# Performance work log

Measured on AMD Instinct MI355X. Metric: run time of the kernel, lower is better.

## Reference

```python
import jax, jax.numpy as jnp
import numpy as np
import math

N_HEADS = 8
D_MODEL = 512
ACTUAL_N = 16
ACTUAL_CH = 64
SEQ = ACTUAL_N * ACTUAL_CH  # 1024
BATCH = 8


def _alibi_slopes(n):
    # n_heads=8 is a power of two, so only the power-of-2 branch is needed
    start = 2.0 ** (-(2.0 ** (-(math.log2(n) - 3))))
    return [start * (start ** i) for i in range(n)]


def setup_inputs() -> dict:
    key = jax.random.key(0)
    ks = jax.random.split(key, 9)
    d = D_MODEL
    w = 0.02  # init scale for weights
    return {
        "Q": jax.random.normal(ks[0], (BATCH, SEQ, d), jnp.float32),
        "Wq": jax.random.normal(ks[1], (d, d), jnp.float32) * w,
        "bq": jnp.zeros((d,), jnp.float32),
        "Wk": jax.random.normal(ks[2], (d, d), jnp.float32) * w,
        "bk": jnp.zeros((d,), jnp.float32),
        "Wv": jax.random.normal(ks[3], (d, d), jnp.float32) * w,
        "bv": jnp.zeros((d,), jnp.float32),
        "Wo": jax.random.normal(ks[4], (d, d), jnp.float32) * w,
        "bo": jnp.zeros((d,), jnp.float32),
        "mask": jnp.ones((SEQ, SEQ), bool),
        "actual_N": ACTUAL_N,
        "actual_ch": ACTUAL_CH,
    }


def reference(Q, Wq, bq, Wk, bk, Wv, bv, Wo, bo, mask, actual_N, actual_ch):
    bs, S, d = Q.shape
    H = N_HEADS
    dk = d // H
    scale = dk ** -0.5  # lsa=False -> frozen scalar

    # QKV projections (K = V = Q, self-attention path), [bs, H, S, dk]
    q = (Q @ Wq.T + bq).reshape(bs, S, H, dk).transpose(0, 2, 1, 3)
    k = (Q @ Wk.T + bk).reshape(bs, S, H, dk).transpose(0, 2, 1, 3)
    v = (Q @ Wv.T + bv).reshape(bs, S, H, dk).transpose(0, 2, 1, 3)

    scores = jnp.einsum('bhqd,bhkd->bhqk', q, k) * scale  # [bs,H,S,S]

    # ALiBi-style bias: per-head slope * tiled (-|i-j|) distance block
    slopes = jnp.asarray(_alibi_slopes(H), jnp.float32)[:, None, None]  # [H,1,1]
    pos = jnp.arange(actual_N)
    dist = (-jnp.abs(pos[:, None] - pos[None, :])).astype(jnp.float32)  # [N,N]
    bias = slopes * jnp.tile(dist, (actual_ch, actual_ch))  # [H,S,S]
    scores = scores + bias

    # mask: True = keep (masked_fill on ~mask)
    scores = jnp.where(mask[None, None, :, :], scores, -jnp.inf)

    attn = jax.nn.softmax(scores, axis=-1)  # dropout=0 (eval)
    out = jnp.einsum('bhqk,bhkd->bhqd', attn, v)  # [bs,H,S,dk]
    out = out.transpose(0, 2, 1, 3).reshape(bs, S, H * dk)
    out = out @ Wo.T + bo
    return (out, attn)
```

## Files before the change

kernel.cpp:

```cpp
#include <hip/hip_runtime.h>
#include <cmath>


namespace {
constexpr int SEQ = 1024;
constexpr int DM  = 512;
constexpr int NH  = 8;
constexpr int DK  = 64;
constexpr float SCALE = 0.125f;
constexpr size_t QKV_ELEMS = (size_t)8 * NH * SEQ * DK;
}

typedef __attribute__((ext_vector_type(8))) short short8_t;
typedef __attribute__((ext_vector_type(4))) float f32x4_t;
typedef __attribute__((ext_vector_type(2))) unsigned u32x2_t;
typedef __attribute__((ext_vector_type(4))) unsigned short ushort4_t;

__device__ inline unsigned bf16h(float x) {
  union { float f; unsigned u; } c; c.f = x;
  return (c.u + 0x7FFFu + ((c.u >> 16) & 1u)) >> 16;
}
__device__ inline float bf16f(unsigned h) {
  union { unsigned u; float f; } c; c.u = h << 16; return c.f;
}

#define GLOAD_LDS16(g, l) __builtin_amdgcn_global_load_lds( \
    (const __attribute__((address_space(1))) void*)(g), \
    (__attribute__((address_space(3))) void*)(l), 16, 0, 0)

__global__ __launch_bounds__(256) void k0_convert(
    const float* __restrict__ X,
    const float* __restrict__ Wq, const float* __restrict__ Wk,
    const float* __restrict__ Wv, const float* __restrict__ Wo,
    unsigned short* __restrict__ Xh, unsigned short* __restrict__ Xl,
    unsigned short* __restrict__ Wh, unsigned short* __restrict__ Wl,
    unsigned short* __restrict__ Woh, unsigned short* __restrict__ Wol)
{
  const size_t gi = ((size_t)blockIdx.x * 256 + threadIdx.x) * 8;
  const float* src; unsigned short* dh; unsigned short* dl; size_t off;
  if (gi < 4194304) { src = X; dh = Xh; dl = Xl; off = gi; }
  else {
    const size_t r = gi - 4194304;
    const int sec = (int)(r >> 18);
    off = r & 262143;
    if (sec == 0)      { src = Wq; dh = Wh;          dl = Wl; }
    else if (sec == 1) { src = Wk; dh = Wh + 262144; dl = Wl + 262144; }
    else if (sec == 2) { src = Wv; dh = Wh + 524288; dl = Wl + 524288; }
    else               { src = Wo; dh = Woh;         dl = Wol; }
  }
  const float4 f0 = *(const float4*)&src[off];
  const float4 f1 = *(const float4*)&src[off + 4];
  const float v[8] = {f0.x, f0.y, f0.z, f0.w, f1.x, f1.y, f1.z, f1.w};
  short8_t hv, lv;
#pragma unroll
  for (int j = 0; j < 8; ++j) {
    const unsigned hh = bf16h(v[j]);
    hv[j] = (short)hh;
    lv[j] = (short)bf16h(v[j] - bf16f(hh));
  }
  *(short8_t*)&dh[off] = hv;
  *(short8_t*)&dl[off] = lv;
}

__device__ inline int swz64(int row, int col16) {
  return row * 64 + (col16 ^ (((row >> 1) & 3) << 4));
}

__global__ __launch_bounds__(256, 3) void k1_gemm(
    const unsigned short* __restrict__ Xh, const unsigned short* __restrict__ Xl,
    const unsigned short* __restrict__ Wh, const unsigned short* __restrict__ Wl,
    const float* __restrict__ bq, const float* __restrict__ bk,
    const float* __restrict__ bv,
    unsigned short* __restrict__ Qh, unsigned short* __restrict__ Ql,
    unsigned short* __restrict__ Kh, unsigned short* __restrict__ Kl,
    unsigned short* __restrict__ VTh, unsigned short* __restrict__ VTl)
{
  const int z = blockIdx.z;
  const int m0 = blockIdx.x * 128, n0 = blockIdx.y * 128;
  const unsigned short* __restrict__ Bph = Wh + (size_t)z * 262144;
  const unsigned short* __restrict__ Bpl = Wl + (size_t)z * 262144;
  const float* bias = (z == 0) ? bq : (z == 1) ? bk : bv;

  __shared__ __align__(16) char sm[32768];

  const int tid = threadIdx.x;
  const int w = tid >> 6, lane = tid & 63, lq = lane & 15, g = lane >> 4;
  const int wm = w >> 1, wn = w & 1;
  const int srow = tid >> 2, schunk = (tid & 3) * 16;

  f32x4_t acc[4][4];
#pragma unroll
  for (int i = 0; i < 4; ++i)
#pragma unroll
    for (int j = 0; j < 4; ++j) acc[i][j] = (f32x4_t){0.f, 0.f, 0.f, 0.f};

  for (int k0 = 0; k0 < DM; k0 += 32) {
    const int kc = k0 + (schunk >> 1);
    const short8_t a0h = *(const short8_t*)&Xh[(size_t)(m0 + srow)      * DM + kc];
    const short8_t a1h = *(const short8_t*)&Xh[(size_t)(m0 + srow + 64) * DM + kc];
    const short8_t a0l = *(const short8_t*)&Xl[(size_t)(m0 + srow)      * DM + kc];
    const short8_t a1l = *(const short8_t*)&Xl[(size_t)(m0 + srow + 64) * DM + kc];
    const short8_t b0h = *(const short8_t*)&Bph[(size_t)(n0 + srow)      * DM + kc];
    const short8_t b1h = *(const short8_t*)&Bph[(size_t)(n0 + srow + 64) * DM + kc];
    const short8_t b0l = *(const short8_t*)&Bpl[(size_t)(n0 + srow)      * DM + kc];
    const short8_t b1l = *(const short8_t*)&Bpl[(size_t)(n0 + srow + 64) * DM + kc];
    __syncthreads();
    *(short8_t*)(sm +         swz64(srow,      schunk)) = a0h;
    *(short8_t*)(sm +         swz64(srow + 64, schunk)) = a1h;
    *(short8_t*)(sm +  8192 + swz64(srow,      schunk)) = a0l;
    *(short8_t*)(sm +  8192 + swz64(srow + 64, schunk)) = a1l;
    *(short8_t*)(sm + 16384 + swz64(srow,      schunk)) = b0h;
    *(short8_t*)(sm + 16384 + swz64(srow + 64, schunk)) = b1h;
    *(short8_t*)(sm + 24576 + swz64(srow,      schunk)) = b0l;
    *(short8_t*)(sm + 24576 + swz64(srow + 64, schunk)) = b1l;
    __syncthreads();

    short8_t ah[4], al[4], bh_[4], bl_[4];
#pragma unroll
    for (int mf = 0; mf < 4; ++mf) {
      const int rowA = wm * 64 + mf * 16 + lq;
      ah[mf] = *(const short8_t*)(sm +        swz64(rowA, g * 16));
      al[mf] = *(const short8_t*)(sm + 8192 + swz64(rowA, g * 16));
    }
#pragma unroll
    for (int nf = 0; nf < 4; ++nf) {
      const int rowB = wn * 64 + nf * 16 + lq;
      bh_[nf] = *(const short8_t*)(sm + 16384 + swz64(rowB, g * 16));
      bl_[nf] = *(const short8_t*)(sm + 24576 + swz64(rowB, g * 16));
    }
#pragma unroll
    for (int mf = 0; mf < 4; ++mf)
#pragma unroll
      for (int nf = 0; nf < 4; ++nf) {
        acc[mf][nf] = __builtin_amdgcn_mfma_f32_16x16x32_bf16(ah[mf], bh_[nf], acc[mf][nf], 0, 0, 0);
        acc[mf][nf] = __builtin_amdgcn_mfma_f32_16x16x32_bf16(al[mf], bh_[nf], acc[mf][nf], 0, 0, 0);
        acc[mf][nf] = __builtin_amdgcn_mfma_f32_16x16x32_bf16(ah[mf], bl_[nf], acc[mf][nf], 0, 0, 0);
      }
  }

  if (z <= 1) {
    unsigned short* Ph = (z == 0) ? Qh : Kh;
    unsigned short* Pl = (z == 0) ? Ql : Kl;
#pragma unroll
    for (int mf = 0; mf < 4; ++mf)
#pragma unroll
      for (int nf = 0; nf < 4; ++nf) {
        const int N = n0 + wn * 64 + nf * 16 + lq;
        const int h = N >> 6, dd = N & 63;
        const float bs = bias[N];
#pragma unroll
        for (int r = 0; r < 4; ++r) {
          const int M = m0 + wm * 64 + mf * 16 + g * 4 + r;
          const int b = M >> 10, s = M & 1023;
          const float val = acc[mf][nf][r] + bs;
          const unsigned hi = bf16h(val);
          const size_t o = ((size_t)((b * 8 + h) * 1024 + s)) * 64 + dd;
          Ph[o] = (unsigned short)hi;
          Pl[o] = (unsigned short)bf16h(val - bf16f(hi));
        }
      }
  } else {
#pragma unroll
    for (int mf = 0; mf < 4; ++mf)
#pragma unroll
      for (int nf = 0; nf < 4; ++nf) {
        const int N = n0 + wn * 64 + nf * 16 + lq;
        const int h = N >> 6, dd = N & 63;
        const float bs = bias[N];
        const int M0 = m0 + wm * 64 + mf * 16 + g * 4;
        const int b = M0 >> 10, s = M0 & 1023;
        ushort4_t hv, lv;
#pragma unroll
        for (int r = 0; r < 4; ++r) {
          const float val = acc[mf][nf][r] + bs;
          const unsigned hi = bf16h(val);
          hv[r] = (unsigned short)hi;
          lv[r] = (unsigned short)bf16h(val - bf16f(hi));
        }
        const size_t o = ((size_t)((b * 8 + h) * 64 + dd)) * 1024 + s;
        *(ushort4_t*)&VTh[o] = hv;
        *(ushort4_t*)&VTl[o] = lv;
      }
  }
}

__global__ __launch_bounds__(512, 2) void k_attn(
    const unsigned short* __restrict__ Qhp, const unsigned short* __restrict__ Qlp,
    const unsigned short* __restrict__ Khp, const unsigned short* __restrict__ Klp,
    const unsigned short* __restrict__ VTh, const unsigned short* __restrict__ VTl,
    float* __restrict__ attn,
    unsigned short* __restrict__ HOh, unsigned short* __restrict__ HOl)
{
  __shared__ __align__(16) char smem[49664];
  float* rsm = (float*)(smem + 49152);

  const int bid = blockIdx.x;
  const int swz = (bid & 7) * 256 + (bid >> 3);
  const int bh = swz >> 5, qt = swz & 31;
  const int hh = bh & 7;
  const float slope = exp2f(-(float)(hh + 1));

  const int tid = threadIdx.x, w = tid >> 6, lane = tid & 63;
  const int lq = lane & 15, g = lane >> 4;
  const int qhalf = w >> 2, kq = w & 3;

  const size_t qkBase = (size_t)bh * (SEQ * DK);

  short8_t qfh[2], qfl[2];
  {
    const size_t qr = qkBase + (size_t)(qt * 32 + qhalf * 16 + lq) * DK;
#pragma unroll
    for (int ks = 0; ks < 2; ++ks) {
      qfh[ks] = *(const short8_t*)&Qhp[qr + ks * 32 + g * 8];
      qfl[ks] = *(const short8_t*)&Qlp[qr + ks * 32 + g * 8];
    }
  }

  float bias[4];
#pragma unroll
  for (int r = 0; r < 4; ++r) {
    const int d = lq - (g * 4 + r);
    bias[r] = -slope * (float)(d < 0 ? -d : d);
  }

  const int srow8 = tid >> 3;
  const int sc    = ((tid & 7) ^ (srow8 & 7)) * 8;

  const int krow = kq * 16 + lq;
  const int kro  = krow * 128;
  const int kc0  = (g ^ (krow & 7)) << 4;
  const int kc1  = ((4 + g) ^ (krow & 7)) << 4;

  f32x4_t e_[16];
  float rs = 0.f;

  {
    const size_t kb0 = qkBase + (size_t)srow8 * DK + sc;
    GLOAD_LDS16(&Khp[kb0], smem + tid * 16);
    GLOAD_LDS16(&Klp[kb0], smem + 8192 + tid * 16);
    const size_t kb1 = qkBase + (size_t)(64 + srow8) * DK + sc;
    GLOAD_LDS16(&Khp[kb1], smem + 16384 + tid * 16);
    GLOAD_LDS16(&Klp[kb1], smem + 16384 + 8192 + tid * 16);
  }

#pragma unroll
  for (int hp = 0; hp < 16; ++hp) {
    if (hp < 15) asm volatile("s_waitcnt vmcnt(2) lgkmcnt(0)" ::: "memory");
    else         asm volatile("s_waitcnt vmcnt(0) lgkmcnt(0)" ::: "memory");
    __builtin_amdgcn_s_barrier();
    __builtin_amdgcn_sched_barrier(0);
    if (hp + 2 < 16) {
      const int b2 = (hp + 2) % 3;
      const size_t kb = qkBase + (size_t)((hp + 2) * 64 + srow8) * DK + sc;
      GLOAD_LDS16(&Khp[kb], smem + b2 * 16384 + tid * 16);
      GLOAD_LDS16(&Klp[kb], smem + b2 * 16384 + 8192 + tid * 16);
    }
    const char* kbuf = smem + (hp % 3) * 16384;
    const short8_t kh0 = *(const short8_t*)(kbuf + kro + kc0);
    const short8_t kh1 = *(const short8_t*)(kbuf + kro + kc1);
    const short8_t kl0 = *(const short8_t*)(kbuf + 8192 + kro + kc0);
    const short8_t kl1 = *(const short8_t*)(kbuf + 8192 + kro + kc1);
    f32x4_t acc = {0.f, 0.f, 0.f, 0.f};
    acc = __builtin_amdgcn_mfma_f32_16x16x32_bf16(kh0, qfh[0], acc, 0, 0, 0);
    acc = __builtin_amdgcn_mfma_f32_16x16x32_bf16(kh1, qfh[1], acc, 0, 0, 0);
    acc = __builtin_amdgcn_mfma_f32_16x16x32_bf16(kl0, qfh[0], acc, 0, 0, 0);
    acc = __builtin_amdgcn_mfma_f32_16x16x32_bf16(kl1, qfh[1], acc, 0, 0, 0);
    acc = __builtin_amdgcn_mfma_f32_16x16x32_bf16(kh0, qfl[0], acc, 0, 0, 0);
    acc = __builtin_amdgcn_mfma_f32_16x16x32_bf16(kh1, qfl[1], acc, 0, 0, 0);
    f32x4_t ee;
#pragma unroll
    for (int r2 = 0; r2 < 4; ++r2) {
      const float x = __expf(fmaf(acc[r2], SCALE, bias[r2]));
      ee[r2] = x;
      rs += x;
    }
    e_[hp] = ee;
  }
  asm volatile("s_waitcnt lgkmcnt(0)" ::: "memory");
  __syncthreads();

  rs += __shfl_xor(rs, 16);
  rs += __shfl_xor(rs, 32);
  if (lane < 16) rsm[w * 16 + lq] = rs;
  __syncthreads();
  const float linv = 1.0f /
      (rsm[(qhalf * 4 + 0) * 16 + lq] + rsm[(qhalf * 4 + 1) * 16 + lq]
     + rsm[(qhalf * 4 + 2) * 16 + lq] + rsm[(qhalf * 4 + 3) * 16 + lq]);

  float* ap = attn + ((size_t)bh << 20) + (size_t)(qt * 32 + qhalf * 16 + lq) * SEQ;
#pragma unroll
  for (int hp = 0; hp < 16; ++hp) {
    f32x4_t a = e_[hp];
    a[0] *= linv; a[1] *= linv; a[2] *= linv; a[3] *= linv;
    e_[hp] = a;
    *(f32x4_t*)&ap[hp * 64 + kq * 16 + g * 4] = a;
  }

  f32x4_t oacc = {0.f, 0.f, 0.f, 0.f};
  const int prow = qhalf * 16 + lq;
  const int brow = kq * 16 + lq;

#pragma unroll
  for (int p = 0; p < 8; ++p) {
    __syncthreads();
#pragma unroll
    for (int r4 = 0; r4 < 4; ++r4) {
      const int dk = (r4 & 1) * 32 + w * 4 + (lane >> 4);
      const int cl = (lane & 15) * 16;
      const unsigned short* vt = (r4 >> 1) ? VTl : VTh;
      const char* src = (const char*)(vt + (size_t)(bh * 64 + dk) * 1024 + p * 128)
                        + (cl ^ ((dk & 7) << 4));
      GLOAD_LDS16(src, smem + r4 * 8192 + w * 1024);
    }
#pragma unroll
    for (int h2 = 0; h2 < 2; ++h2) {
      const f32x4_t ee = e_[2 * p + h2];
      const unsigned u0 = bf16h(ee[0]) | (bf16h(ee[1]) << 16);
      const unsigned u1 = bf16h(ee[2]) | (bf16h(ee[3]) << 16);
      const int byte = 32768 + prow * 256
                     + ((h2 * 128 + kq * 32 + g * 8) ^ ((prow & 7) << 4));
      *(u32x2_t*)(smem + byte) = (u32x2_t){u0, u1};
    }
    __syncthreads();
#pragma unroll
    for (int cs = 0; cs < 4; ++cs) {
      const int cb = cs * 64 + g * 16;
      const short8_t pa = *(const short8_t*)(smem + 32768 + prow * 256 + (cb ^ ((prow & 7) << 4)));
      const short8_t vh = *(const short8_t*)(smem +         brow * 256 + (cb ^ ((brow & 7) << 4)));
      const short8_t vl = *(const short8_t*)(smem + 16384 + brow * 256 + (cb ^ ((brow & 7) << 4)));
      oacc = __builtin_amdgcn_mfma_f32_16x16x32_bf16(pa, vh, oacc, 0, 0, 0);
      oacc = __builtin_amdgcn_mfma_f32_16x16x32_bf16(pa, vl, oacc, 0, 0, 0);
    }
  }

  {
    const int dk = kq * 16 + lq;
#pragma unroll
    for (int r = 0; r < 4; ++r) {
      const int srow = qt * 32 + qhalf * 16 + g * 4 + r;
      const float val = oacc[r];
      const unsigned hi = bf16h(val);
      const size_t o = ((size_t)(bh * 1024 + srow)) * 64 + dk;
      HOh[o] = (unsigned short)hi;
      HOl[o] = (unsigned short)bf16h(val - bf16f(hi));
    }
  }
}

__global__ __launch_bounds__(256, 3) void k4_gemm(
    const unsigned short* __restrict__ Ahp, const unsigned short* __restrict__ Alp,
    const unsigned short* __restrict__ Bph, const unsigned short* __restrict__ Bpl,
    const float* __restrict__ bo, float* __restrict__ out)
{
  const int m0 = blockIdx.x * 128, n0 = blockIdx.y * 128;

  __shared__ __align__(16) char sm[32768];

  const int tid = threadIdx.x;
  const int w = tid >> 6, lane = tid & 63, lq = lane & 15, g = lane >> 4;
  const int wm = w >> 1, wn = w & 1;
  const int srow = tid >> 2, schunk = (tid & 3) * 16;

  f32x4_t acc[4][4];
#pragma unroll
  for (int i = 0; i < 4; ++i)
#pragma unroll
    for (int j = 0; j < 4; ++j) acc[i][j] = (f32x4_t){0.f, 0.f, 0.f, 0.f};

  for (int k0 = 0; k0 < DM; k0 += 32) {
    const int kk = k0 + (schunk >> 1);
    const int h = kk >> 6, dd = kk & 63;
    const int Ma = m0 + srow, Mb = m0 + srow + 64;
    const size_t oa = ((size_t)((Ma >> 10) * 8 + h) * 1024 + (Ma & 1023)) * 64 + dd;
    const size_t ob = ((size_t)((Mb >> 10) * 8 + h) * 1024 + (Mb & 1023)) * 64 + dd;
    const short8_t a0h = *(const short8_t*)&Ahp[oa];
    const short8_t a1h = *(const short8_t*)&Ahp[ob];
    const short8_t a0l = *(const short8_t*)&Alp[oa];
    const short8_t a1l = *(const short8_t*)&Alp[ob];
    const short8_t b0h = *(const short8_t*)&Bph[(size_t)(n0 + srow)      * DM + kk];
    const short8_t b1h = *(const short8_t*)&Bph[(size_t)(n0 + srow + 64) * DM + kk];
    const short8_t b0l = *(const short8_t*)&Bpl[(size_t)(n0 + srow)      * DM + kk];
    const short8_t b1l = *(const short8_t*)&Bpl[(size_t)(n0 + srow + 64) * DM + kk];
    __syncthreads();
    *(short8_t*)(sm +         swz64(srow,      schunk)) = a0h;
    *(short8_t*)(sm +         swz64(srow + 64, schunk)) = a1h;
    *(short8_t*)(sm +  8192 + swz64(srow,      schunk)) = a0l;
    *(short8_t*)(sm +  8192 + swz64(srow + 64, schunk)) = a1l;
    *(short8_t*)(sm + 16384 + swz64(srow,      schunk)) = b0h;
    *(short8_t*)(sm + 16384 + swz64(srow + 64, schunk)) = b1h;
    *(short8_t*)(sm + 24576 + swz64(srow,      schunk)) = b0l;
    *(short8_t*)(sm + 24576 + swz64(srow + 64, schunk)) = b1l;
    __syncthreads();

    short8_t ah[4], al[4], bh_[4], bl_[4];
#pragma unroll
    for (int mf = 0; mf < 4; ++mf) {
      const int rowA = wm * 64 + mf * 16 + lq;
      ah[mf] = *(const short8_t*)(sm +        swz64(rowA, g * 16));
      al[mf] = *(const short8_t*)(sm + 8192 + swz64(rowA, g * 16));
    }
#pragma unroll
    for (int nf = 0; nf < 4; ++nf) {
      const int rowB = wn * 64 + nf * 16 + lq;
      bh_[nf] = *(const short8_t*)(sm + 16384 + swz64(rowB, g * 16));
      bl_[nf] = *(const short8_t*)(sm + 24576 + swz64(rowB, g * 16));
    }
#pragma unroll
    for (int mf = 0; mf < 4; ++mf)
#pragma unroll
      for (int nf = 0; nf < 4; ++nf) {
        acc[mf][nf] = __builtin_amdgcn_mfma_f32_16x16x32_bf16(ah[mf], bh_[nf], acc[mf][nf], 0, 0, 0);
        acc[mf][nf] = __builtin_amdgcn_mfma_f32_16x16x32_bf16(al[mf], bh_[nf], acc[mf][nf], 0, 0, 0);
        acc[mf][nf] = __builtin_amdgcn_mfma_f32_16x16x32_bf16(ah[mf], bl_[nf], acc[mf][nf], 0, 0, 0);
      }
  }

#pragma unroll
  for (int mf = 0; mf < 4; ++mf)
#pragma unroll
    for (int nf = 0; nf < 4; ++nf) {
      const int N = n0 + wn * 64 + nf * 16 + lq;
      const float bs = bo[N];
#pragma unroll
      for (int r = 0; r < 4; ++r) {
        const int M = m0 + wm * 64 + mf * 16 + g * 4 + r;
        out[(size_t)M * DM + N] = acc[mf][nf][r] + bs;
      }
    }
}

extern "C" void kernel_launch(void* const* d_in, const int* in_sizes, int n_in,
                              void* d_out, int out_size, void* d_ws, size_t ws_size,
                              hipStream_t stream) {
  (void)in_sizes; (void)n_in; (void)out_size; (void)ws_size;
  const float* X  = (const float*)d_in[0];
  const float* Wq = (const float*)d_in[1];
  const float* bq = (const float*)d_in[2];
  const float* Wk = (const float*)d_in[3];
  const float* bk = (const float*)d_in[4];
  const float* Wv = (const float*)d_in[5];
  const float* bv = (const float*)d_in[6];
  const float* Wo = (const float*)d_in[7];
  const float* bo = (const float*)d_in[8];

  float* out  = (float*)d_out;
  float* attn = out + QKV_ELEMS;

  unsigned short* Xh  = (unsigned short*)d_ws;
  unsigned short* Xl  = Xh  + 4194304;
  unsigned short* Wh  = Xl  + 4194304;
  unsigned short* Wl  = Wh  + 786432;
  unsigned short* Woh = Wl  + 786432;
  unsigned short* Wol = Woh + 262144;
  unsigned short* Qh  = Wol + 262144;
  unsigned short* Ql  = Qh  + 4194304;
  unsigned short* Kh  = Ql  + 4194304;
  unsigned short* Kl  = Kh  + 4194304;
  unsigned short* VTh = Kl  + 4194304;
  unsigned short* VTl = VTh + 4194304;
  unsigned short* HOh = Xh;
  unsigned short* HOl = Xl;

  k0_convert<<<dim3(2560),    256, 0, stream>>>(X, Wq, Wk, Wv, Wo,
                                                Xh, Xl, Wh, Wl, Woh, Wol);
  k1_gemm  <<<dim3(64, 4, 3), 256, 0, stream>>>(Xh, Xl, Wh, Wl, bq, bk, bv,
                                                Qh, Ql, Kh, Kl, VTh, VTl);
  k_attn   <<<dim3(2048),     512, 0, stream>>>(Qh, Ql, Kh, Kl, VTh, VTl,
                                                attn, HOh, HOl);
  k4_gemm  <<<dim3(64, 4),    256, 0, stream>>>(HOh, HOl, Woh, Wol, bo, out);
}
```

Before: 197.5 us.

## Triple-buffer V tiles and double-buffer P in attention PV loop

```diff
diff --git a/kernel.cpp b/kernel.cpp
--- a/kernel.cpp
+++ b/kernel.cpp
@@ -191,8 +191,8 @@
     float* __restrict__ attn,
     unsigned short* __restrict__ HOh, unsigned short* __restrict__ HOl)
 {
-  __shared__ __align__(16) char smem[49664];
-  float* rsm = (float*)(smem + 49152);
+  __shared__ __align__(16) char smem[57856];
+  float* rsm = (float*)(smem + 57344);
 
   const int bid = blockIdx.x;
   const int swz = (bid & 7) * 256 + (bid >> 3);
@@ -286,51 +286,63 @@
   const float linv = 1.0f /
       (rsm[(qhalf * 4 + 0) * 16 + lq] + rsm[(qhalf * 4 + 1) * 16 + lq]
      + rsm[(qhalf * 4 + 2) * 16 + lq] + rsm[(qhalf * 4 + 3) * 16 + lq]);
-
-  float* ap = attn + ((size_t)bh << 20) + (size_t)(qt * 32 + qhalf * 16 + lq) * SEQ;
 #pragma unroll
   for (int hp = 0; hp < 16; ++hp) {
-    f32x4_t a = e_[hp];
-    a[0] *= linv; a[1] *= linv; a[2] *= linv; a[3] *= linv;
-    e_[hp] = a;
-    *(f32x4_t*)&ap[hp * 64 + kq * 16 + g * 4] = a;
+    e_[hp][0] *= linv; e_[hp][1] *= linv;
+    e_[hp][2] *= linv; e_[hp][3] *= linv;
   }
 
   f32x4_t oacc = {0.f, 0.f, 0.f, 0.f};
   const int prow = qhalf * 16 + lq;
   const int brow = kq * 16 + lq;
-
-#pragma unroll
-  for (int p = 0; p < 8; ++p) {
-    __syncthreads();
-#pragma unroll
-    for (int r4 = 0; r4 < 4; ++r4) {
-      const int dk = (r4 & 1) * 32 + w * 4 + (lane >> 4);
-      const int cl = (lane & 15) * 16;
-      const unsigned short* vt = (r4 >> 1) ? VTl : VTh;
-      const char* src = (const char*)(vt + (size_t)(bh * 64 + dk) * 1024 + p * 128)
-                        + (cl ^ ((dk & 7) << 4));
-      GLOAD_LDS16(src, smem + r4 * 8192 + w * 1024);
-    }
-#pragma unroll
-    for (int h2 = 0; h2 < 2; ++h2) {
-      const f32x4_t ee = e_[2 * p + h2];
-      const unsigned u0 = bf16h(ee[0]) | (bf16h(ee[1]) << 16);
-      const unsigned u1 = bf16h(ee[2]) | (bf16h(ee[3]) << 16);
-      const int byte = 32768 + prow * 256
-                     + ((h2 * 128 + kq * 32 + g * 8) ^ ((prow & 7) << 4));
-      *(u32x2_t*)(smem + byte) = (u32x2_t){u0, u1};
-    }
-    __syncthreads();
-#pragma unroll
-    for (int cs = 0; cs < 4; ++cs) {
-      const int cb = cs * 64 + g * 16;
-      const short8_t pa = *(const short8_t*)(smem + 32768 + prow * 256 + (cb ^ ((prow & 7) << 4)));
-      const short8_t vh = *(const short8_t*)(smem +         brow * 256 + (cb ^ ((brow & 7) << 4)));
-      const short8_t vl = *(const short8_t*)(smem + 16384 + brow * 256 + (cb ^ ((brow & 7) << 4)));
-      oacc = __builtin_amdgcn_mfma_f32_16x16x32_bf16(pa, vh, oacc, 0, 0, 0);
-      oacc = __builtin_amdgcn_mfma_f32_16x16x32_bf16(pa, vl, oacc, 0, 0, 0);
-    }
+  const int pwofs = 49152 + prow * 128 + ((kq * 32 + g * 8) ^ ((prow & 7) << 4));
+  const int prd0 = 49152 + prow * 128 + ((g * 16) ^ ((prow & 7) << 4));
+  const int prd1 = 49152 + prow * 128 + ((64 + g * 16) ^ ((prow & 7) << 4));
+  const int vrd0 = brow * 128 + ((g * 16) ^ ((brow & 7) << 4));
+  const int vrd1 = brow * 128 + ((64 + g * 16) ^ ((brow & 7) << 4));
+
+  {
+    const size_t vb = (size_t)(bh * 64 + srow8) * 1024 + sc;
+    GLOAD_LDS16(&VTh[vb],      smem + tid * 16);
+    GLOAD_LDS16(&VTl[vb],      smem + 8192 + tid * 16);
+    GLOAD_LDS16(&VTh[vb + 64], smem + 16384 + tid * 16);
+    GLOAD_LDS16(&VTl[vb + 64], smem + 16384 + 8192 + tid * 16);
+    const f32x4_t e0 = e_[0];
+    *(u32x2_t*)(smem + pwofs) = (u32x2_t){
+        bf16h(e0[0]) | (bf16h(e0[1]) << 16),
+        bf16h(e0[2]) | (bf16h(e0[3]) << 16)};
+  }
+
+#pragma unroll
+  for (int hp = 0; hp < 16; ++hp) {
+    if (hp < 15) asm volatile("s_waitcnt vmcnt(2) lgkmcnt(0)" ::: "memory");
+    else         asm volatile("s_waitcnt vmcnt(0) lgkmcnt(0)" ::: "memory");
+    __builtin_amdgcn_s_barrier();
+    __builtin_amdgcn_sched_barrier(0);
+    if (hp + 2 < 16) {
+      const int b2 = (hp + 2) % 3;
+      const size_t vb = (size_t)(bh * 64 + srow8) * 1024 + (hp + 2) * 64 + sc;
+      GLOAD_LDS16(&VTh[vb], smem + b2 * 16384 + tid * 16);
+      GLOAD_LDS16(&VTl[vb], smem + b2 * 16384 + 8192 + tid * 16);
+    }
+    if (hp + 1 < 16) {
+      const f32x4_t en = e_[hp + 1];
+      *(u32x2_t*)(smem + ((hp + 1) & 1) * 4096 + pwofs) = (u32x2_t){
+          bf16h(en[0]) | (bf16h(en[1]) << 16),
+          bf16h(en[2]) | (bf16h(en[3]) << 16)};
+    }
+    const char* vbuf = smem + (hp % 3) * 16384;
+    const int pb = (hp & 1) * 4096;
+    const short8_t pa0 = *(const short8_t*)(smem + pb + prd0);
+    const short8_t pa1 = *(const short8_t*)(smem + pb + prd1);
+    const short8_t vh0 = *(const short8_t*)(vbuf + vrd0);
+    const short8_t vh1 = *(const short8_t*)(vbuf + vrd1);
+    const short8_t vl0 = *(const short8_t*)(vbuf + 8192 + vrd0);
+    const short8_t vl1 = *(const short8_t*)(vbuf + 8192 + vrd1);
+    oacc = __builtin_amdgcn_mfma_f32_16x16x32_bf16(pa0, vh0, oacc, 0, 0, 0);
+    oacc = __builtin_amdgcn_mfma_f32_16x16x32_bf16(pa0, vl0, oacc, 0, 0, 0);
+    oacc = __builtin_amdgcn_mfma_f32_16x16x32_bf16(pa1, vh1, oacc, 0, 0, 0);
+    oacc = __builtin_amdgcn_mfma_f32_16x16x32_bf16(pa1, vl1, oacc, 0, 0, 0);
   }
 
   {
@@ -344,6 +356,14 @@
       HOh[o] = (unsigned short)hi;
       HOl[o] = (unsigned short)bf16h(val - bf16f(hi));
     }
+  }
+
+  {
+    float* ap = attn + ((size_t)bh << 20)
+              + (size_t)(qt * 32 + qhalf * 16 + lq) * SEQ;
+#pragma unroll
+    for (int hp = 0; hp < 16; ++hp)
+      *(f32x4_t*)&ap[hp * 64 + kq * 16 + g * 4] = e_[hp];
   }
 }
 
```

Result: faster. 182.9 us (-7.4%).
